# Performance work log

Measured on AMD Instinct MI355X. Metric: run time of the kernel, lower is better.

## Reference

```python
import jax, jax.numpy as jnp
import numpy as np

N, E, F_IN, H, G = 100000, 3200000, 128, 256, 64


def gcn_layer(x, src, dst, W, b, n):
    # GCNConv with added self-loops and symmetric normalization:
    # out = D^{-1/2} (A + I) D^{-1/2} X W + b
    h = x @ W  # [n, H]
    deg = jax.ops.segment_sum(jnp.ones_like(dst, dtype=h.dtype), dst, num_segments=n) + 1.0
    dinv = jax.lax.rsqrt(deg)
    coef = dinv[src] * dinv[dst]  # [E]
    agg = jax.ops.segment_sum(h[src] * coef[:, None], dst, num_segments=n)
    out = agg + h * (dinv * dinv)[:, None]  # self-loop term: 1/deg
    return out + b


def global_mean_pool(x, batch, num_graphs):
    sums = jax.ops.segment_sum(x, batch, num_segments=num_graphs)
    cnts = jax.ops.segment_sum(jnp.ones((x.shape[0],), x.dtype), batch, num_segments=num_graphs)
    return sums / jnp.maximum(cnts, 1.0)[:, None]


def conv_pass(x, edge_index, batch, params):
    (W0, b0, W1, b1, W2, b2, lin0_W, lin0_b) = params
    src, dst = edge_index[0], edge_index[1]
    n = x.shape[0]
    x = jax.nn.relu(gcn_layer(x, src, dst, W0, b0, n))
    x = jax.nn.relu(gcn_layer(x, src, dst, W1, b1, n))
    x = gcn_layer(x, src, dst, W2, b2, n)
    x = global_mean_pool(x, batch, G)
    # dropout(p=0.5) is identity in eval mode
    return x @ lin0_W + lin0_b  # [G, H/2]


def setup_inputs() -> dict:
    key = jax.random.key(0)
    ks = jax.random.split(key, 20)
    d = {}
    for i, nm in enumerate(['x0', 'x1', 'x2']):
        d[nm] = jax.random.normal(ks[i], (N, F_IN), dtype=jnp.float32)
    for i, nm in enumerate(['edge_index0', 'edge_index1', 'edge_index2']):
        d[nm] = jax.random.randint(ks[3 + i], (2, E), 0, N, dtype=jnp.int32)
    for i, nm in enumerate(['batch0', 'batch1', 'batch2']):
        d[nm] = jnp.sort(jax.random.randint(ks[6 + i], (N,), 0, G, dtype=jnp.int32))
    s = lambda fan: 1.0 / np.sqrt(fan)
    d['W0'] = jax.random.uniform(ks[9], (F_IN, H), jnp.float32, -s(F_IN), s(F_IN))
    d['b0'] = jnp.zeros((H,), jnp.float32)
    d['W1'] = jax.random.uniform(ks[10], (H, H), jnp.float32, -s(H), s(H))
    d['b1'] = jnp.zeros((H,), jnp.float32)
    d['W2'] = jax.random.uniform(ks[11], (H, H), jnp.float32, -s(H), s(H))
    d['b2'] = jnp.zeros((H,), jnp.float32)
    d['lin0_W'] = jax.random.uniform(ks[12], (H, H // 2), jnp.float32, -s(H), s(H))
    d['lin0_b'] = jax.random.uniform(ks[13], (H // 2,), jnp.float32, -s(H), s(H))
    d['lin_W'] = jax.random.uniform(ks[14], (H, 1), jnp.float32, -s(H), s(H))
    d['lin_b'] = jax.random.uniform(ks[15], (1,), jnp.float32, -s(H), s(H))
    return d


def reference(x0, x1, x2, edge_index0, edge_index1, edge_index2,
              batch0, batch1, batch2,
              W0, b0, W1, b1, W2, b2, lin0_W, lin0_b, lin_W, lin_b):
    params = (W0, b0, W1, b1, W2, b2, lin0_W, lin0_b)
    z0 = conv_pass(x0, edge_index0, batch0, params)
    z1 = conv_pass(x1, edge_index1, batch1, params)
    z2 = conv_pass(x2, edge_index2, batch2, params)
    EPS = 1e-6  # torch F.pairwise_distance eps
    dist_p = jnp.linalg.norm(z0 - z1 + EPS, axis=1)
    dist_n = jnp.linalg.norm(z0 - z2 + EPS, axis=1)
    y1 = jnp.concatenate([z0, z1], axis=1) @ lin_W + lin_b
    y2 = jnp.concatenate([z0, z2], axis=1) @ lin_W + lin_b
    score_p = jax.nn.sigmoid(y1)
    score_n = jax.nn.sigmoid(y2)
    correct = jnp.sum(dist_n - dist_p > 0).astype(jnp.int32).reshape(1)
    correct_score = jnp.sum(score_p - score_n > 0).astype(jnp.int32).reshape(1)
    return (z0, z1, z2, correct, score_p, score_n, correct_score)
```

## Files before the change

### kernel.cpp

```cpp
#include <hip/hip_runtime.h>
#include <math.h>

#define NN 100000
#define EE 3200000

typedef __attribute__((ext_vector_type(8))) short bf16x8;
typedef __attribute__((ext_vector_type(4))) float f32x4;

__device__ __forceinline__ unsigned short f2b(float f) {
  unsigned u = __float_as_uint(f);
  u += 0x7fffu + ((u >> 16) & 1u);
  return (unsigned short)(u >> 16);
}
__device__ __forceinline__ float b2f(unsigned short s) {
  return __uint_as_float(((unsigned)s) << 16);
}
__device__ __forceinline__ float blo(unsigned u) { return __uint_as_float(u << 16); }
__device__ __forceinline__ float bhi(unsigned u) { return __uint_as_float(u & 0xffff0000u); }
__device__ __forceinline__ unsigned pack2(float lo, float hi) {
  return ((unsigned)f2b(hi) << 16) | (unsigned)f2b(lo);
}

__global__ void zero_int(int* __restrict__ p, int n) {
  int i = blockIdx.x * 256 + threadIdx.x;
  if (i < n) p[i] = 0;
}

__global__ void hist_deg3(const int* __restrict__ d0, const int* __restrict__ d1,
                          const int* __restrict__ d2, int* __restrict__ deg3, int e) {
  int i = blockIdx.x * 256 + threadIdx.x;
  if (i >= e) return;
  const int* dst = (blockIdx.y == 0) ? d0 : (blockIdx.y == 1) ? d1 : d2;
  atomicAdd(&deg3[blockIdx.y * NN + dst[i]], 1);
}

__global__ void calc_dinv3(const int* __restrict__ deg3, float* __restrict__ dinv3, int n3) {
  int i = blockIdx.x * 256 + threadIdx.x;
  if (i < n3) dinv3[i] = 1.0f / sqrtf((float)(deg3[i] + 1));
}

__global__ __launch_bounds__(1024) void scan_excl3(const int* __restrict__ deg3,
                                                   int* __restrict__ offs3, int n) {
  const int* deg = deg3 + blockIdx.x * NN;
  int* offs = offs3 + blockIdx.x * (NN + 1);
  __shared__ int wsum[16];
  __shared__ int s_carry;
  int tid = threadIdx.x;
  int lane = tid & 63, wv = tid >> 6;
  if (tid == 0) s_carry = 0;
  __syncthreads();
  for (int base = 0; base < n; base += 1024) {
    int idx = base + tid;
    int v = (idx < n) ? deg[idx] : 0;
    int x = v;
#pragma unroll
    for (int o = 1; o < 64; o <<= 1) {
      int t = __shfl_up(x, o, 64);
      if (lane >= o) x += t;
    }
    if (lane == 63) wsum[wv] = x;
    __syncthreads();
    int carry = s_carry;
    int woff = 0;
    for (int j = 0; j < wv; ++j) woff += wsum[j];
    if (idx < n) offs[idx] = carry + woff + x - v;
    __syncthreads();
    if (tid == 1023) s_carry = carry + woff + x;
    __syncthreads();
  }
  if (threadIdx.x == 0) offs[n] = s_carry;
}

__global__ void fill_csr(const int* __restrict__ src, const int* __restrict__ dst,
                         const float* __restrict__ dinv, const int* __restrict__ offs,
                         int* __restrict__ fillc, unsigned long long* __restrict__ ent,
                         int e) {
  int i = blockIdx.x * 256 + threadIdx.x;
  if (i >= e) return;
  int d = dst[i], s = src[i];
  int pos = offs[d] + atomicAdd(&fillc[d], 1);
  unsigned long long w = (unsigned long long)(unsigned)__float_as_int(dinv[s]);
  ent[pos] = (w << 32) | (unsigned)s;
}

__global__ void conv_bf(const float* __restrict__ in, unsigned* __restrict__ out, int n4) {
  int i = blockIdx.x * 256 + threadIdx.x;
  if (i >= n4) return;
  float4 v = ((const float4*)in)[i];
  ((uint2*)out)[i] = make_uint2(pack2(v.x, v.y), pack2(v.z, v.w));
}

__global__ void conv_wt(const float* __restrict__ W, unsigned short* __restrict__ Wt, int K) {
  int i = blockIdx.x * 256 + threadIdx.x;
  if (i >= 256 * K) return;
  int nn = i / K, kk = i - nn * K;
  Wt[i] = f2b(W[(size_t)kk * 256 + nn]);
}

__global__ __launch_bounds__(256) void agg256_bf(const unsigned short* __restrict__ x,
    const unsigned long long* __restrict__ ent, const int* __restrict__ offs,
    const float* __restrict__ dinv, unsigned short* __restrict__ y, int n) {
  int v = (blockIdx.x * 256 + threadIdx.x) >> 6;
  v = __builtin_amdgcn_readfirstlane(v);
  int lane = threadIdx.x & 63;
  if (v >= n) return;
  float dv = dinv[v];
  const uint2* selfp = (const uint2*)(x + ((size_t)(unsigned)v << 8)) + lane;
  uint2 self = *selfp;
  float a0 = dv * blo(self.x), a1 = dv * bhi(self.x);
  float a2 = dv * blo(self.y), a3 = dv * bhi(self.y);
  int s = offs[v], e = offs[v + 1];
  int i = s;
  for (; i + 3 < e; i += 4) {
    unsigned long long p0 = ent[i], p1 = ent[i + 1], p2 = ent[i + 2], p3 = ent[i + 3];
    unsigned s0 = (unsigned)p0, s1 = (unsigned)p1, s2 = (unsigned)p2, s3 = (unsigned)p3;
    float w0 = __uint_as_float((unsigned)(p0 >> 32));
    float w1 = __uint_as_float((unsigned)(p1 >> 32));
    float w2 = __uint_as_float((unsigned)(p2 >> 32));
    float w3 = __uint_as_float((unsigned)(p3 >> 32));
    uint2 r0 = *((const uint2*)(x + ((size_t)s0 << 8)) + lane);
    uint2 r1 = *((const uint2*)(x + ((size_t)s1 << 8)) + lane);
    uint2 r2 = *((const uint2*)(x + ((size_t)s2 << 8)) + lane);
    uint2 r3 = *((const uint2*)(x + ((size_t)s3 << 8)) + lane);
    a0 += w0 * blo(r0.x); a1 += w0 * bhi(r0.x); a2 += w0 * blo(r0.y); a3 += w0 * bhi(r0.y);
    a0 += w1 * blo(r1.x); a1 += w1 * bhi(r1.x); a2 += w1 * blo(r1.y); a3 += w1 * bhi(r1.y);
    a0 += w2 * blo(r2.x); a1 += w2 * bhi(r2.x); a2 += w2 * blo(r2.y); a3 += w2 * bhi(r2.y);
    a0 += w3 * blo(r3.x); a1 += w3 * bhi(r3.x); a2 += w3 * blo(r3.y); a3 += w3 * bhi(r3.y);
  }
  for (; i < e; ++i) {
    unsigned long long p0 = ent[i];
    unsigned s0 = (unsigned)p0;
    float w0 = __uint_as_float((unsigned)(p0 >> 32));
    uint2 r0 = *((const uint2*)(x + ((size_t)s0 << 8)) + lane);
    a0 += w0 * blo(r0.x); a1 += w0 * bhi(r0.x); a2 += w0 * blo(r0.y); a3 += w0 * bhi(r0.y);
  }
  uint2* yp = (uint2*)(y + ((size_t)(unsigned)v << 8)) + lane;
  *yp = make_uint2(pack2(dv * a0, dv * a1), pack2(dv * a2, dv * a3));
}

__global__ __launch_bounds__(256) void agg128_bf(const unsigned short* __restrict__ x,
    const unsigned long long* __restrict__ ent, const int* __restrict__ offs,
    const float* __restrict__ dinv, unsigned short* __restrict__ y, int n) {
  int v = (blockIdx.x * 256 + threadIdx.x) >> 6;
  v = __builtin_amdgcn_readfirstlane(v);
  int lane = threadIdx.x & 63;
  if (v >= n) return;
  float dv = dinv[v];
  const unsigned* selfp = (const unsigned*)(x + ((size_t)(unsigned)v << 7)) + lane;
  unsigned self = *selfp;
  float a0 = dv * blo(self), a1 = dv * bhi(self);
  int s = offs[v], e = offs[v + 1];
  int i = s;
  for (; i + 3 < e; i += 4) {
    unsigned long long p0 = ent[i], p1 = ent[i + 1], p2 = ent[i + 2], p3 = ent[i + 3];
    unsigned s0 = (unsigned)p0, s1 = (unsigned)p1, s2 = (unsigned)p2, s3 = (unsigned)p3;
    float w0 = __uint_as_float((unsigned)(p0 >> 32));
    float w1 = __uint_as_float((unsigned)(p1 >> 32));
    float w2 = __uint_as_float((unsigned)(p2 >> 32));
    float w3 = __uint_as_float((unsigned)(p3 >> 32));
    unsigned r0 = *((const unsigned*)(x + ((size_t)s0 << 7)) + lane);
    unsigned r1 = *((const unsigned*)(x + ((size_t)s1 << 7)) + lane);
    unsigned r2 = *((const unsigned*)(x + ((size_t)s2 << 7)) + lane);
    unsigned r3 = *((const unsigned*)(x + ((size_t)s3 << 7)) + lane);
    a0 += w0 * blo(r0); a1 += w0 * bhi(r0);
    a0 += w1 * blo(r1); a1 += w1 * bhi(r1);
    a0 += w2 * blo(r2); a1 += w2 * bhi(r2);
    a0 += w3 * blo(r3); a1 += w3 * bhi(r3);
  }
  for (; i < e; ++i) {
    unsigned long long p0 = ent[i];
    unsigned s0 = (unsigned)p0;
    float w0 = __uint_as_float((unsigned)(p0 >> 32));
    unsigned r0 = *((const unsigned*)(x + ((size_t)s0 << 7)) + lane);
    a0 += w0 * blo(r0); a1 += w0 * bhi(r0);
  }
  unsigned* yp = (unsigned*)(y + ((size_t)(unsigned)v << 7)) + lane;
  *yp = pack2(dv * a0, dv * a1);
}

#define LDA 40
__global__ __launch_bounds__(256) void gemm_mfma(
    const unsigned short* __restrict__ A, const unsigned short* __restrict__ Bt,
    const float* __restrict__ bias, unsigned short* __restrict__ C,
    int M, int K, int do_relu) {
  __shared__ unsigned short As[128 * LDA];
  __shared__ unsigned short Bs[128 * LDA];
  int tid = threadIdx.x;
  int row0 = blockIdx.x * 128;
  int col0 = blockIdx.y * 128;
  int wave = tid >> 6, lane = tid & 63;
  int wm = wave >> 1, wn = wave & 1;
  int lr = lane & 15, quad = lane >> 4;

  f32x4 acc[4][4];
#pragma unroll
  for (int i = 0; i < 4; ++i)
#pragma unroll
    for (int j = 0; j < 4; ++j) acc[i][j] = (f32x4){0.f, 0.f, 0.f, 0.f};

  for (int k0 = 0; k0 < K; k0 += 32) {
#pragma unroll
    for (int p = 0; p < 2; ++p) {
      int i = tid + p * 256;
      int r = i >> 2, q = i & 3;
      int row = row0 + r; if (row >= M) row = M - 1;
      uint4 va = *(const uint4*)(A + (size_t)row * K + k0 + q * 8);
      *(uint4*)&As[r * LDA + q * 8] = va;
      uint4 vb = *(const uint4*)(Bt + (size_t)(col0 + r) * K + k0 + q * 8);
      *(uint4*)&Bs[r * LDA + q * 8] = vb;
    }
    __syncthreads();
    bf16x8 af[4], bf[4];
#pragma unroll
    for (int mi = 0; mi < 4; ++mi)
      af[mi] = *(const bf16x8*)&As[(wm * 64 + mi * 16 + lr) * LDA + quad * 8];
#pragma unroll
    for (int ni = 0; ni < 4; ++ni)
      bf[ni] = *(const bf16x8*)&Bs[(wn * 64 + ni * 16 + lr) * LDA + quad * 8];
#pragma unroll
    for (int mi = 0; mi < 4; ++mi)
#pragma unroll
      for (int ni = 0; ni < 4; ++ni)
        acc[mi][ni] = __builtin_amdgcn_mfma_f32_16x16x32_bf16(af[mi], bf[ni], acc[mi][ni], 0, 0, 0);
    __syncthreads();
  }

  float bv[4];
#pragma unroll
  for (int ni = 0; ni < 4; ++ni) bv[ni] = bias[col0 + wn * 64 + ni * 16 + lr];
#pragma unroll
  for (int mi = 0; mi < 4; ++mi) {
#pragma unroll
    for (int r = 0; r < 4; ++r) {
      int grow = row0 + wm * 64 + mi * 16 + quad * 4 + r;
      if (grow < M) {
#pragma unroll
        for (int ni = 0; ni < 4; ++ni) {
          float v = acc[mi][ni][r] + bv[ni];
          if (do_relu) v = fmaxf(v, 0.f);
          C[(size_t)grow * 256 + col0 + wn * 64 + ni * 16 + lr] = f2b(v);
        }
      }
    }
  }
}

__global__ __launch_bounds__(256) void pool_sum_bf(const unsigned short* __restrict__ h,
    const int* __restrict__ batch, float* __restrict__ sums,
    float* __restrict__ cnts, int n) {
  int f = threadIdx.x;
  int v0 = blockIdx.x * 128;
  if (v0 >= n) return;
  int vend = min(v0 + 128, n);
  int cur = batch[v0];
  float acc = 0.f;
  int cnt = 0;
  for (int v = v0; v < vend; ++v) {
    int b = batch[v];
    if (b != cur) {
      atomicAdd(&sums[cur * 256 + f], acc);
      if (f == 0) atomicAdd(&cnts[cur], (float)cnt);
      acc = 0.f; cnt = 0; cur = b;
    }
    acc += b2f(h[(size_t)v * 256 + f]);
    cnt++;
  }
  atomicAdd(&sums[cur * 256 + f], acc);
  if (f == 0) atomicAdd(&cnts[cur], (float)cnt);
}

__global__ __launch_bounds__(128) void pool_lin(const float* __restrict__ sums,
    const float* __restrict__ cnts, const float* __restrict__ W128,
    const float* __restrict__ b128, float* __restrict__ z) {
  int g = blockIdx.x, f = threadIdx.x;
  float inv = 1.0f / fmaxf(cnts[g], 1.0f);
  float acc = 0.f;
  for (int k = 0; k < 256; ++k)
    acc += (sums[g * 256 + k] * inv) * W128[k * 128 + f];
  z[g * 128 + f] = acc + b128[f];
}

__global__ __launch_bounds__(64) void final_triplet(const float* __restrict__ z,
    const float* __restrict__ lin_W, const float* __restrict__ lin_b,
    float* __restrict__ out) {
  int g = threadIdx.x;
  const float* z0 = z;
  const float* z1 = z + 8192;
  const float* z2 = z + 16384;
  float dp = 0.f, dn = 0.f;
  float y1 = lin_b[0], y2 = lin_b[0];
  for (int f = 0; f < 128; ++f) {
    float a = z0[g * 128 + f], b = z1[g * 128 + f], c = z2[g * 128 + f];
    float d1 = a - b + 1e-6f, d2 = a - c + 1e-6f;
    dp += d1 * d1; dn += d2 * d2;
    float w0 = lin_W[f], w1 = lin_W[128 + f];
    y1 += a * w0 + b * w1;
    y2 += a * w0 + c * w1;
  }
  dp = sqrtf(dp); dn = sqrtf(dn);
  float sp = 1.f / (1.f + expf(-y1));
  float sn = 1.f / (1.f + expf(-y2));
  out[24577 + g] = sp;
  out[24641 + g] = sn;
  unsigned long long m1 = __ballot(dn - dp > 0.f);
  unsigned long long m2 = __ballot(sp - sn > 0.f);
  if (g == 0) {
    out[24576] = (float)__popcll(m1);
    out[24705] = (float)__popcll(m2);
  }
}

extern "C" void kernel_launch(void* const* d_in, const int* in_sizes, int n_in,
                              void* d_out, int out_size, void* d_ws, size_t ws_size,
                              hipStream_t stream) {
  const float* xin[3]  = {(const float*)d_in[0], (const float*)d_in[1], (const float*)d_in[2]};
  const int* ei[3]     = {(const int*)d_in[3], (const int*)d_in[4], (const int*)d_in[5]};
  const int* batch[3]  = {(const int*)d_in[6], (const int*)d_in[7], (const int*)d_in[8]};
  const float* W0 = (const float*)d_in[9],  *b0 = (const float*)d_in[10];
  const float* W1 = (const float*)d_in[11], *b1 = (const float*)d_in[12];
  const float* W2 = (const float*)d_in[13], *b2 = (const float*)d_in[14];
  const float* lin0W = (const float*)d_in[15], *lin0b = (const float*)d_in[16];
  const float* linW  = (const float*)d_in[17], *linb  = (const float*)d_in[18];
  float* out = (float*)d_out;

  unsigned short* ybf = (unsigned short*)d_ws;
  unsigned short* hbf = ybf + (size_t)NN * 256;
  unsigned short* xbf = hbf + (size_t)NN * 256;
  unsigned long long* ent = (unsigned long long*)(xbf + (size_t)NN * 128);
  unsigned short* Wt0 = (unsigned short*)(ent + EE);
  unsigned short* Wt1 = Wt0 + 256 * 128;
  unsigned short* Wt2 = Wt1 + 256 * 256;
  int* deg3   = (int*)(Wt2 + 256 * 256);
  int* fillc3 = deg3 + 3 * NN;
  float* sums3 = (float*)(fillc3 + 3 * NN);
  float* cnts3 = sums3 + 3 * 64 * 256;
  int zero_elems = 3 * NN + 3 * NN + 3 * 64 * 256 + 3 * 64;
  float* dinv3 = cnts3 + 3 * 64;
  int* offs3 = (int*)(dinv3 + 3 * NN);

  const int EB = (EE + 255) / 256;
  dim3 ggrid((NN + 127) / 128, 2);

  conv_wt<<<(256 * 128 + 255) / 256, 256, 0, stream>>>(W0, Wt0, 128);
  conv_wt<<<(256 * 256 + 255) / 256, 256, 0, stream>>>(W1, Wt1, 256);
  conv_wt<<<(256 * 256 + 255) / 256, 256, 0, stream>>>(W2, Wt2, 256);

  zero_int<<<(zero_elems + 255) / 256, 256, 0, stream>>>(deg3, zero_elems);
  hist_deg3<<<dim3(EB, 3), 256, 0, stream>>>(ei[0] + EE, ei[1] + EE, ei[2] + EE, deg3, EE);
  calc_dinv3<<<(3 * NN + 255) / 256, 256, 0, stream>>>(deg3, dinv3, 3 * NN);
  scan_excl3<<<3, 1024, 0, stream>>>(deg3, offs3, NN);

  for (int g = 0; g < 3; ++g) {
    const int* src = ei[g];
    const int* dst = ei[g] + EE;
    const float* dinv = dinv3 + (size_t)g * NN;
    const int* offs = offs3 + (size_t)g * (NN + 1);

    fill_csr<<<EB, 256, 0, stream>>>(src, dst, dinv, offs, fillc3 + (size_t)g * NN, ent, EE);

    conv_bf<<<(NN * 128 / 4 + 255) / 256, 256, 0, stream>>>(xin[g], (unsigned*)xbf, NN * 128 / 4);

    agg128_bf<<<(NN + 3) / 4, 256, 0, stream>>>(xbf, ent, offs, dinv, ybf, NN);
    gemm_mfma<<<ggrid, 256, 0, stream>>>(ybf, Wt0, b0, hbf, NN, 128, 1);
    agg256_bf<<<(NN + 3) / 4, 256, 0, stream>>>(hbf, ent, offs, dinv, ybf, NN);
    gemm_mfma<<<ggrid, 256, 0, stream>>>(ybf, Wt1, b1, hbf, NN, 256, 1);
    agg256_bf<<<(NN + 3) / 4, 256, 0, stream>>>(hbf, ent, offs, dinv, ybf, NN);
    gemm_mfma<<<ggrid, 256, 0, stream>>>(ybf, Wt2, b2, hbf, NN, 256, 0);

    pool_sum_bf<<<(NN + 127) / 128, 256, 0, stream>>>(hbf, batch[g],
        sums3 + (size_t)g * 64 * 256, cnts3 + (size_t)g * 64, NN);
    pool_lin<<<64, 128, 0, stream>>>(sums3 + (size_t)g * 64 * 256, cnts3 + (size_t)g * 64,
        lin0W, lin0b, out + g * 8192);
  }

  final_triplet<<<1, 64, 0, stream>>>(out, linW, linb, out);
}
```

Before: 3.352 ms.

## Replace global-atomic degree histogram and single-block scan with LDS-privatized histogram and decoupled scan

Computes node in-degrees with per-block LDS histograms packed as 16-bit counters, over 7 node-range passes and 16 edge slices, followed by a reduction kernel. This replaces 9.6M global atomics. The serial 3-block exclusive scan becomes a three-phase parallel scan (chunk sums, mid scan, final). The aim is to remove global-atomic contention and the serial scan latency. The cost is that every pass rereads all edges, and the 16-bit counters can overflow if an in-degree exceeds 65535.

```diff
diff --git a/kernel.cpp b/kernel.cpp
--- a/kernel.cpp
+++ b/kernel.cpp
@@ -21,54 +21,116 @@
   return ((unsigned)f2b(hi) << 16) | (unsigned)f2b(lo);
 }
 
+#define WPB 8192
+#define NODES_PER_PASS 16384
+#define NPASS 7
+#define HB 16
+
 __global__ void zero_int(int* __restrict__ p, int n) {
   int i = blockIdx.x * 256 + threadIdx.x;
   if (i < n) p[i] = 0;
 }
 
-__global__ void hist_deg3(const int* __restrict__ d0, const int* __restrict__ d1,
-                          const int* __restrict__ d2, int* __restrict__ deg3, int e) {
-  int i = blockIdx.x * 256 + threadIdx.x;
-  if (i >= e) return;
-  const int* dst = (blockIdx.y == 0) ? d0 : (blockIdx.y == 1) ? d1 : d2;
-  atomicAdd(&deg3[blockIdx.y * NN + dst[i]], 1);
-}
-
-__global__ void calc_dinv3(const int* __restrict__ deg3, float* __restrict__ dinv3, int n3) {
-  int i = blockIdx.x * 256 + threadIdx.x;
-  if (i < n3) dinv3[i] = 1.0f / sqrtf((float)(deg3[i] + 1));
-}
-
-__global__ __launch_bounds__(1024) void scan_excl3(const int* __restrict__ deg3,
-                                                   int* __restrict__ offs3, int n) {
-  const int* deg = deg3 + blockIdx.x * NN;
-  int* offs = offs3 + blockIdx.x * (NN + 1);
-  __shared__ int wsum[16];
-  __shared__ int s_carry;
-  int tid = threadIdx.x;
-  int lane = tid & 63, wv = tid >> 6;
-  if (tid == 0) s_carry = 0;
+__global__ __launch_bounds__(256) void hist_part(
+    const int* __restrict__ d0, const int* __restrict__ d1, const int* __restrict__ d2,
+    unsigned* __restrict__ partials) {
+  __shared__ unsigned cnt[WPB];
+  int b = blockIdx.x, p = blockIdx.y, g = blockIdx.z;
+  const int* dst = (g == 0) ? d0 : (g == 1) ? d1 : d2;
+  for (int i = threadIdx.x; i < WPB; i += 256) cnt[i] = 0;
   __syncthreads();
-  for (int base = 0; base < n; base += 1024) {
-    int idx = base + tid;
-    int v = (idx < n) ? deg[idx] : 0;
-    int x = v;
-#pragma unroll
-    for (int o = 1; o < 64; o <<= 1) {
-      int t = __shfl_up(x, o, 64);
-      if (lane >= o) x += t;
-    }
-    if (lane == 63) wsum[wv] = x;
-    __syncthreads();
-    int carry = s_carry;
-    int woff = 0;
-    for (int j = 0; j < wv; ++j) woff += wsum[j];
-    if (idx < n) offs[idx] = carry + woff + x - v;
-    __syncthreads();
-    if (tid == 1023) s_carry = carry + woff + x;
-    __syncthreads();
-  }
-  if (threadIdx.x == 0) offs[n] = s_carry;
+  unsigned lo = (unsigned)(p * NODES_PER_PASS);
+  int base = b * (EE / HB);
+  int end = base + EE / HB;
+  for (int i = base + threadIdx.x; i < end; i += 256) {
+    unsigned n = (unsigned)dst[i] - lo;
+    if (n < NODES_PER_PASS)
+      atomicAdd(&cnt[n >> 1], 1u << ((n & 1) * 16));
+  }
+  __syncthreads();
+  unsigned* out = partials + ((size_t)((g * NPASS + p) * HB + b)) * WPB;
+  for (int i = threadIdx.x; i < WPB; i += 256) out[i] = cnt[i];
+}
+
+__global__ void hist_reduce(const unsigned* __restrict__ partials,
+                            unsigned* __restrict__ deg3w) {
+  int i = blockIdx.x * 256 + threadIdx.x;
+  int p = blockIdx.y, g = blockIdx.z;
+  unsigned s = 0;
+  const unsigned* base = partials + ((size_t)((g * NPASS + p) * HB)) * WPB + i;
+#pragma unroll
+  for (int b = 0; b < HB; ++b) s += base[(size_t)b * WPB];
+  int word = p * WPB + i;
+  if (word < NN / 2) deg3w[(size_t)g * (NN / 2) + word] = s;
+}
+
+__global__ void calc_dinv3(const unsigned short* __restrict__ deg3u,
+                           float* __restrict__ dinv3, int n3) {
+  int i = blockIdx.x * 256 + threadIdx.x;
+  if (i < n3) dinv3[i] = 1.0f / sqrtf((float)(deg3u[i] + 1));
+}
+
+#define SCHUNK 1024
+#define NCHUNK 98
+
+__global__ __launch_bounds__(256) void scan_part(const unsigned short* __restrict__ deg3u,
+                                                 int* __restrict__ bsum) {
+  int c = blockIdx.x, g = blockIdx.y;
+  const unsigned short* deg = deg3u + (size_t)g * NN;
+  int base = c * SCHUNK;
+  int s = 0;
+  for (int i = threadIdx.x; i < SCHUNK; i += 256) {
+    int idx = base + i;
+    s += (idx < NN) ? (int)deg[idx] : 0;
+  }
+#pragma unroll
+  for (int o = 32; o; o >>= 1) s += __shfl_down(s, o, 64);
+  __shared__ int ws[4];
+  if ((threadIdx.x & 63) == 0) ws[threadIdx.x >> 6] = s;
+  __syncthreads();
+  if (threadIdx.x == 0) bsum[g * NCHUNK + c] = ws[0] + ws[1] + ws[2] + ws[3];
+}
+
+__global__ __launch_bounds__(128) void scan_mid(int* __restrict__ bsum) {
+  int g = blockIdx.x;
+  int t = threadIdx.x;
+  int v = (t < NCHUNK) ? bsum[g * NCHUNK + t] : 0;
+  int lane = t & 63, wv = t >> 6;
+  int x = v;
+#pragma unroll
+  for (int o = 1; o < 64; o <<= 1) {
+    int tt = __shfl_up(x, o, 64);
+    if (lane >= o) x += tt;
+  }
+  __shared__ int w0sum;
+  if (wv == 0 && lane == 63) w0sum = x;
+  __syncthreads();
+  int excl = x - v + (wv ? w0sum : 0);
+  if (t < NCHUNK) bsum[g * NCHUNK + t] = excl;
+}
+
+__global__ __launch_bounds__(1024) void scan_final(const unsigned short* __restrict__ deg3u,
+    const int* __restrict__ bsum, int* __restrict__ offs3) {
+  int c = blockIdx.x, g = blockIdx.y;
+  const unsigned short* deg = deg3u + (size_t)g * NN;
+  int* offs = offs3 + (size_t)g * (NN + 1);
+  int t = threadIdx.x;
+  int idx = c * SCHUNK + t;
+  int v = (idx < NN) ? (int)deg[idx] : 0;
+  int lane = t & 63, wv = t >> 6;
+  int x = v;
+#pragma unroll
+  for (int o = 1; o < 64; o <<= 1) {
+    int tt = __shfl_up(x, o, 64);
+    if (lane >= o) x += tt;
+  }
+  __shared__ int ws[16];
+  if (lane == 63) ws[wv] = x;
+  __syncthreads();
+  int woff = 0;
+  for (int j = 0; j < wv; ++j) woff += ws[j];
+  if (idx < NN) offs[idx] = bsum[g * NCHUNK + c] + woff + x - v;
+  if (idx == NN - 1) offs[NN] = EE;
 }
 
 __global__ void fill_csr(const int* __restrict__ src, const int* __restrict__ dst,
@@ -330,13 +392,16 @@
   unsigned short* Wt0 = (unsigned short*)(ent + EE);
   unsigned short* Wt1 = Wt0 + 256 * 128;
   unsigned short* Wt2 = Wt1 + 256 * 256;
-  int* deg3   = (int*)(Wt2 + 256 * 256);
-  int* fillc3 = deg3 + 3 * NN;
+  int* fillc3 = (int*)(Wt2 + 256 * 256);
   float* sums3 = (float*)(fillc3 + 3 * NN);
   float* cnts3 = sums3 + 3 * 64 * 256;
-  int zero_elems = 3 * NN + 3 * NN + 3 * 64 * 256 + 3 * 64;
+  int zero_elems = 3 * NN + 3 * 64 * 256 + 3 * 64;
   float* dinv3 = cnts3 + 3 * 64;
   int* offs3 = (int*)(dinv3 + 3 * NN);
+  unsigned* deg3w = (unsigned*)(offs3 + 3 * (NN + 1));
+  int* bsum = (int*)(deg3w + 3 * (NN / 2));
+  unsigned* partials = (unsigned*)(bsum + 3 * NCHUNK);
+  const unsigned short* deg3u = (const unsigned short*)deg3w;
 
   const int EB = (EE + 255) / 256;
   dim3 ggrid((NN + 127) / 128, 2);
@@ -345,10 +410,13 @@
   conv_wt<<<(256 * 256 + 255) / 256, 256, 0, stream>>>(W1, Wt1, 256);
   conv_wt<<<(256 * 256 + 255) / 256, 256, 0, stream>>>(W2, Wt2, 256);
 
-  zero_int<<<(zero_elems + 255) / 256, 256, 0, stream>>>(deg3, zero_elems);
-  hist_deg3<<<dim3(EB, 3), 256, 0, stream>>>(ei[0] + EE, ei[1] + EE, ei[2] + EE, deg3, EE);
-  calc_dinv3<<<(3 * NN + 255) / 256, 256, 0, stream>>>(deg3, dinv3, 3 * NN);
-  scan_excl3<<<3, 1024, 0, stream>>>(deg3, offs3, NN);
+  zero_int<<<(zero_elems + 255) / 256, 256, 0, stream>>>(fillc3, zero_elems);
+  hist_part<<<dim3(HB, NPASS, 3), 256, 0, stream>>>(ei[0] + EE, ei[1] + EE, ei[2] + EE, partials);
+  hist_reduce<<<dim3(WPB / 256, NPASS, 3), 256, 0, stream>>>(partials, deg3w);
+  calc_dinv3<<<(3 * NN + 255) / 256, 256, 0, stream>>>(deg3u, dinv3, 3 * NN);
+  scan_part<<<dim3(NCHUNK, 3), 256, 0, stream>>>(deg3u, bsum);
+  scan_mid<<<3, 128, 0, stream>>>(bsum);
+  scan_final<<<dim3(NCHUNK, 3), 1024, 0, stream>>>(deg3u, bsum, offs3);
 
   for (int g = 0; g < 3; ++g) {
     const int* src = ei[g];
```

Result: faster. 3.237 ms (-3.5%).
